# Performance work log

Hardware: AMD Instinct MI355X
Metric: run time of the kernel (lower is better)

The kernel has to match this reference:

```python
import jax, jax.numpy as jnp
import numpy as np

# Mamba2 config fixed by the wrapper: state=32, expand=1, n_groups=1, conv kernel=4
H, P, N, K = 32, 64, 32, 4          # heads, head_dim, state_size, conv kernel
D_MODEL = H * P                      # hidden = intermediate (expand=1) = 2048
CONV_DIM = D_MODEL + 2 * N           # intermediate + 2*n_groups*state = 2112
PROJ = D_MODEL + CONV_DIM + H        # in_proj width = 4192
EPS = 1e-6


def setup_inputs() -> dict:
    key = jax.random.key(0)
    ks = jax.random.split(key, 8)
    B, L = 4, 2048
    w = lambda k, shape, sc=0.02: jax.random.normal(k, shape, jnp.float32) * sc
    return {
        "x": jax.random.normal(ks[0], (B, L, D_MODEL), jnp.float32),
        "W_in": w(ks[1], (D_MODEL, PROJ)),
        "b_in": jnp.zeros((PROJ,), jnp.float32),
        "conv_w": w(ks[2], (CONV_DIM, K), 0.25),
        "conv_b": jnp.zeros((CONV_DIM,), jnp.float32),
        "A_log": jnp.log(jnp.arange(1, H + 1, dtype=jnp.float32)),
        "dt_bias": jax.random.uniform(ks[3], (H,), jnp.float32, -4.0, 0.0),
        "D_param": jnp.ones((H,), jnp.float32),
        "norm_w": jnp.ones((D_MODEL,), jnp.float32),
        "W_out": w(ks[4], (D_MODEL, D_MODEL)),
    }


def reference(x, W_in, b_in, conv_w, conv_b, A_log, dt_bias, D_param, norm_w, W_out):
    B, L, _ = x.shape
    proj = x @ W_in + b_in                                   # (B,L,PROJ)
    gate, hBC, dt_raw = jnp.split(proj, [D_MODEL, D_MODEL + CONV_DIM], axis=-1)

    # causal depthwise conv1d over time (kernel K, left pad K-1), then SiLU
    hp = jnp.pad(hBC, ((0, 0), (K - 1, 0), (0, 0)))
    conv = conv_b + sum(hp[:, k:k + L, :] * conv_w[:, k] for k in range(K))
    conv = jax.nn.silu(conv)

    xs, Bm, Cm = jnp.split(conv, [D_MODEL, D_MODEL + N], axis=-1)
    xs = xs.reshape(B, L, H, P)                              # (B,L,H,P)

    A = -jnp.exp(A_log)                                      # (H,)
    dt = jax.nn.softplus(dt_raw + dt_bias)                   # (B,L,H)
    dA = jnp.exp(dt * A)                                     # (B,L,H)

    def step(hstate, inp):
        dA_t, dt_t, x_t, B_t, C_t = inp                      # (B,H),(B,H),(B,H,P),(B,N),(B,N)
        upd = (dt_t[:, :, None] * x_t)[..., None] * B_t[:, None, None, :]
        hstate = dA_t[:, :, None, None] * hstate + upd       # (B,H,P,N)
        y_t = jnp.einsum('bhpn,bn->bhp', hstate, C_t)
        return hstate, y_t

    h0 = jnp.zeros((B, H, P, N), x.dtype)
    scan_in = (dA.transpose(1, 0, 2), dt.transpose(1, 0, 2),
               xs.transpose(1, 0, 2, 3), Bm.transpose(1, 0, 2), Cm.transpose(1, 0, 2))
    _, ys = jax.lax.scan(step, h0, scan_in)                  # ys: (L,B,H,P)

    y = ys.transpose(1, 0, 2, 3) + D_param[None, None, :, None] * xs
    y = y.reshape(B, L, D_MODEL)

    # gated RMSNorm: gate applied before normalization (MambaRMSNormGated)
    y = y * jax.nn.silu(gate)
    var = jnp.mean(jnp.square(y), axis=-1, keepdims=True)
    y = y * jax.lax.rsqrt(var + EPS) * norm_w
    return y @ W_out
```

## Files before the change

kernel.cpp:

```cpp
#include <hip/hip_runtime.h>
#include <cstdint>
#include <cstddef>

constexpr int kB    = 4;
constexpr int kL    = 2048;
constexpr int kH    = 32;
constexpr int kP    = 64;
constexpr int kN    = 32;
constexpr int kD    = 2048;
constexpr int kProjW = 4192;
constexpr int kLdp  = 4224;
constexpr int kNp1  = 4352;
constexpr int kM    = kB * kL;
constexpr int kK    = kD;
constexpr int kLC   = 128;
constexpr int kNC   = kL / kLC;

typedef _Float16 f16x8 __attribute__((ext_vector_type(8)));
typedef float f32x4 __attribute__((ext_vector_type(4)));

__device__ __forceinline__ float lane_bcast(float v, int lane) {
    return __int_as_float(__builtin_amdgcn_readlane(__float_as_int(v), lane));
}
__device__ __forceinline__ float silu_f(float x) { return x / (1.f + __expf(-x)); }

__device__ __forceinline__ void async_copy16(const void* g, void* lds) {
    __builtin_amdgcn_global_load_lds(
        (const __attribute__((address_space(1))) unsigned int*)(uintptr_t)g,
        (__attribute__((address_space(3))) unsigned int*)(uintptr_t)lds,
        16, 0, 0);
}

__global__ __launch_bounds__(256) void cast_f16_kernel(const float* __restrict__ in,
                                                       _Float16* __restrict__ out) {
    size_t i = ((size_t)blockIdx.x * 256 + threadIdx.x) * 8;
    float4 a = *(const float4*)(in + i);
    float4 b = *(const float4*)(in + i + 4);
    f16x8 o;
    o[0] = (_Float16)a.x; o[1] = (_Float16)a.y; o[2] = (_Float16)a.z; o[3] = (_Float16)a.w;
    o[4] = (_Float16)b.x; o[5] = (_Float16)b.y; o[6] = (_Float16)b.z; o[7] = (_Float16)b.w;
    *(f16x8*)(out + i) = o;
}

__global__ __launch_bounds__(256) void transpose_cast_kernel(const float* __restrict__ W,
                                                             _Float16* __restrict__ Wt,
                                                             int R, int C) {
    __shared__ float tile[32][33];
    const int c0 = blockIdx.x * 32;
    const int r0 = blockIdx.y * 32;
    const int tx = threadIdx.x & 31;
    const int ty = threadIdx.x >> 5;
    #pragma unroll
    for (int i = 0; i < 32; i += 8) {
        int rr = r0 + ty + i;
        int cc = c0 + tx;
        tile[ty + i][tx] = (cc < C) ? W[(size_t)rr * C + cc] : 0.f;
    }
    __syncthreads();
    #pragma unroll
    for (int i = 0; i < 32; i += 8) {
        int cc = c0 + ty + i;
        int rr = r0 + tx;
        Wt[(size_t)cc * R + rr] = (_Float16)tile[tx][ty + i];
    }
}

template <bool OUT_F16>
__global__ __launch_bounds__(512, 2) void gemm256_kernel(
    const _Float16* __restrict__ A, const _Float16* __restrict__ Bt,
    const float* __restrict__ bias, int nbias,
    void* __restrict__ Cout, int K, int ldc, int nvalid, int nn,
    float* __restrict__ dtside)
{
    __shared__ __attribute__((aligned(16))) _Float16 lds[2 * 4 * 8192];

    const int tid = threadIdx.x;
    const int l = tid & 63, r = l & 15, q = l >> 4;
    const int w = tid >> 6, wm = w >> 2, wn = w & 3;

    const int nwg = gridDim.x;
    const int q8 = nwg >> 3;
    const int pid = blockIdx.x;
    const int wg = (pid & 7) * q8 + (pid >> 3);
    const int m_idx = wg / nn;
    const int n_idx = wg - m_idx * nn;
    const size_t tileM = (size_t)m_idx * 256;
    const size_t tileN = (size_t)n_idx * 256;

    const int sR = ((tid >> 7) << 4) | (tid & 15);
    const int sC = ((tid >> 4) & 7) << 3;
    const _Float16* aSrc = A  + (tileM + sR) * (size_t)K + sC;
    const _Float16* bSrc = Bt + (tileN + sR) * (size_t)K + sC;
    _Float16* dst0 = lds + tid * 8;

    auto STAGE = [&](int buf, int part, const _Float16* src, int half, int kt2) {
        const _Float16* s = src + (size_t)(half * 128) * K + kt2 * 64;
        _Float16* d = dst0 + buf * 32768 + part * 8192;
        async_copy16(s, d);
        async_copy16(s + (size_t)64 * K, d + 4096);
    };

    const int NT = K >> 6;
    STAGE(0, 0, aSrc, 0, 0); STAGE(0, 3, bSrc, 1, 0);
    STAGE(0, 1, aSrc, 1, 0); STAGE(0, 2, bSrc, 0, 0);
    STAGE(1, 0, aSrc, 0, 1); STAGE(1, 3, bSrc, 1, 1);
    STAGE(1, 1, aSrc, 1, 1);
    asm volatile("s_waitcnt vmcnt(6)" ::: "memory");
    asm volatile("s_barrier" ::: "memory");

    f32x4 acc[8][4] = {};
    f16x8 afr[4][2], bfr[2][2], bfr2[2][2];

    const int aRd = wm * 4 * 2048 + l * 16;
    const int bRd = wn * 2 * 2048 + l * 16;

#define MFMA_CL(AO, BO, BARR, KK)                                                        \
    _Pragma("unroll")                                                                    \
    for (int i = 0; i < 4; ++i)                                                          \
        _Pragma("unroll")                                                                \
        for (int j = 0; j < 2; ++j)                                                      \
            acc[(AO) + i][(BO) + j] = __builtin_amdgcn_mfma_f32_16x16x32_f16(            \
                afr[i][KK], BARR[j][KK], acc[(AO) + i][(BO) + j], 0, 0, 0);

    for (int kt = 0; kt < NT; ++kt) {
        const int bsel = kt & 1;
        const char* a0 = (const char*)lds + bsel * 65536;
        const char* a1 = a0 + 16384;
        const char* b0 = a0 + 2 * 16384;
        const char* b1 = a0 + 3 * 16384;

        bfr[0][0] = *(const f16x8*)(b0 + bRd);
        bfr[1][0] = *(const f16x8*)(b0 + bRd + 2048);
        afr[0][0] = *(const f16x8*)(a0 + aRd);
        afr[1][0] = *(const f16x8*)(a0 + aRd + 2048);
        afr[2][0] = *(const f16x8*)(a0 + aRd + 4096);
        afr[3][0] = *(const f16x8*)(a0 + aRd + 6144);
        bfr[0][1] = *(const f16x8*)(b0 + bRd + 1024);
        bfr[1][1] = *(const f16x8*)(b0 + bRd + 3072);
        afr[0][1] = *(const f16x8*)(a0 + aRd + 1024);
        afr[1][1] = *(const f16x8*)(a0 + aRd + 3072);
        afr[2][1] = *(const f16x8*)(a0 + aRd + 5120);
        afr[3][1] = *(const f16x8*)(a0 + aRd + 7168);
        if (kt + 1 < NT) STAGE(bsel ^ 1, 2, bSrc, 0, kt + 1);
        asm volatile("s_waitcnt lgkmcnt(6)" ::: "memory");
        __builtin_amdgcn_sched_barrier(0);
        __builtin_amdgcn_s_setprio(1);
        MFMA_CL(0, 0, bfr, 0)
        asm volatile("s_waitcnt lgkmcnt(0)" ::: "memory");
        __builtin_amdgcn_sched_barrier(0);
        MFMA_CL(0, 0, bfr, 1)
        __builtin_amdgcn_s_setprio(0);
        asm volatile("s_barrier" ::: "memory");

        bfr2[0][0] = *(const f16x8*)(b1 + bRd);
        bfr2[1][0] = *(const f16x8*)(b1 + bRd + 2048);
        bfr2[0][1] = *(const f16x8*)(b1 + bRd + 1024);
        bfr2[1][1] = *(const f16x8*)(b1 + bRd + 3072);
        if (kt + 2 < NT) STAGE(bsel, 0, aSrc, 0, kt + 2);
        asm volatile("s_waitcnt lgkmcnt(2)" ::: "memory");
        __builtin_amdgcn_sched_barrier(0);
        __builtin_amdgcn_s_setprio(1);
        MFMA_CL(0, 2, bfr2, 0)
        asm volatile("s_waitcnt lgkmcnt(0)" ::: "memory");
        __builtin_amdgcn_sched_barrier(0);
        MFMA_CL(0, 2, bfr2, 1)
        __builtin_amdgcn_s_setprio(0);
        asm volatile("s_barrier" ::: "memory");

        afr[0][0] = *(const f16x8*)(a1 + aRd);
        afr[1][0] = *(const f16x8*)(a1 + aRd + 2048);
        afr[2][0] = *(const f16x8*)(a1 + aRd + 4096);
        afr[3][0] = *(const f16x8*)(a1 + aRd + 6144);
        afr[0][1] = *(const f16x8*)(a1 + aRd + 1024);
        afr[1][1] = *(const f16x8*)(a1 + aRd + 3072);
        afr[2][1] = *(const f16x8*)(a1 + aRd + 5120);
        afr[3][1] = *(const f16x8*)(a1 + aRd + 7168);
        if (kt + 2 < NT) STAGE(bsel, 3, bSrc, 1, kt + 2);
        asm volatile("s_waitcnt lgkmcnt(4)" ::: "memory");
        __builtin_amdgcn_sched_barrier(0);
        __builtin_amdgcn_s_setprio(1);
        MFMA_CL(4, 2, bfr2, 0)
        asm volatile("s_waitcnt lgkmcnt(0)" ::: "memory");
        __builtin_amdgcn_sched_barrier(0);
        MFMA_CL(4, 2, bfr2, 1)
        __builtin_amdgcn_s_setprio(0);
        asm volatile("s_barrier" ::: "memory");

        if (kt + 2 < NT) STAGE(bsel, 1, aSrc, 1, kt + 2);
        __builtin_amdgcn_s_setprio(1);
        MFMA_CL(4, 0, bfr, 0)
        MFMA_CL(4, 0, bfr, 1)
        __builtin_amdgcn_s_setprio(0);
        if (kt + 2 < NT) asm volatile("s_waitcnt vmcnt(6)" ::: "memory");
        else             asm volatile("s_waitcnt vmcnt(0)" ::: "memory");
        asm volatile("s_barrier" ::: "memory");
    }
#undef MFMA_CL

    #pragma unroll
    for (int bb = 0; bb < 4; ++bb) {
        const int nh = bb >> 1, j = bb & 1;
        const int col = (int)tileN + nh * 128 + wn * 32 + j * 16 + r;
        if (col >= nvalid) continue;
        float bv = 0.f;
        if (bias != nullptr && col < nbias) bv = bias[col];
        #pragma unroll
        for (int aa = 0; aa < 8; ++aa) {
            const int mh = aa >> 2, i = aa & 3;
            const size_t row = tileM + (size_t)(mh * 128 + wm * 64 + i * 16 + q * 4);
            #pragma unroll
            for (int u = 0; u < 4; ++u) {
                float v = acc[aa][bb][u] + bv;
                if (OUT_F16) ((_Float16*)Cout)[(row + u) * (size_t)ldc + col] = (_Float16)v;
                else         ((float*)Cout)[(row + u) * (size_t)ldc + col] = v;
                if (dtside != nullptr && col >= 4160 && col < 4192)
                    dtside[(row + u) * 32 + (col - 4160)] = v;
            }
        }
    }
}

__global__ __launch_bounds__(256) void dt_da_kernel(
    const float* __restrict__ dtraw, const float* __restrict__ A_log,
    const float* __restrict__ dt_bias, float* __restrict__ dtv, float* __restrict__ dAv)
{
    int idx = blockIdx.x * 256 + threadIdx.x;
    int t  = idx & (kL - 1);
    int bh = idx >> 11;
    int h  = bh & (kH - 1);
    int b  = bh >> 5;
    float z  = dtraw[((size_t)(b * kL + t)) * kH + h] + dt_bias[h];
    float dt = (z > 20.f) ? z : log1pf(expf(z));
    float dA = expf(dt * -expf(A_log[h]));
    dtv[idx] = dt;
    dAv[idx] = dA;
}

__global__ __launch_bounds__(64) void scan_pass1_kernel(
    const _Float16* __restrict__ projh, const float* __restrict__ conv_w,
    const float* __restrict__ conv_b, const float* __restrict__ dtv,
    const float* __restrict__ dAv, float* __restrict__ cstate, float* __restrict__ Pch)
{
    const int blk = blockIdx.x;
    const int c   = blk & (kNC - 1);
    const int bh  = blk >> 4;
    const int h   = bh & (kH - 1);
    const int b   = bh >> 5;
    const int l   = threadIdx.x;
    const int t0  = c * kLC;

    const int chx = h * kP + l;
    const int chb = 2048 + (l & 31);
    const float xw0 = conv_w[chx*4+0], xw1 = conv_w[chx*4+1], xw2 = conv_w[chx*4+2], xw3 = conv_w[chx*4+3];
    const float xbb = conv_b[chx];
    const float bw0 = conv_w[chb*4+0], bw1 = conv_w[chb*4+1], bw2 = conv_w[chb*4+2], bw3 = conv_w[chb*4+3];
    const float bbb = conv_b[chb];

    const _Float16* pb = projh + (size_t)b * kL * kLdp;
    const int colx = 2048 + chx;
    const int colb = 2048 + chb;

    float xq0=0.f, xq1=0.f, xq2=0.f, bq0=0.f, bq1=0.f, bq2=0.f;
    if (c > 0) {
        xq0 = (float)pb[(size_t)(t0-3)*kLdp + colx];
        xq1 = (float)pb[(size_t)(t0-2)*kLdp + colx];
        xq2 = (float)pb[(size_t)(t0-1)*kLdp + colx];
        bq0 = (float)pb[(size_t)(t0-3)*kLdp + colb];
        bq1 = (float)pb[(size_t)(t0-2)*kLdp + colb];
        bq2 = (float)pb[(size_t)(t0-1)*kLdp + colb];
    }

    float hs[kN];
    #pragma unroll
    for (int n = 0; n < kN; ++n) hs[n] = 0.f;
    float Pp = 1.f;
    const float* dtp = dtv + (size_t)bh * kL;
    const float* dAp = dAv + (size_t)bh * kL;

    #pragma unroll 1
    for (int t = t0; t < t0 + kLC; ++t) {
        const size_t ro = (size_t)t * kLdp;
        float xv = (float)pb[ro + colx];
        float bv = (float)pb[ro + colb];
        float sx = silu_f(xbb + xw0*xq0 + xw1*xq1 + xw2*xq2 + xw3*xv);
        float sb = silu_f(bbb + bw0*bq0 + bw1*bq1 + bw2*bq2 + bw3*bv);
        xq0=xq1; xq1=xq2; xq2=xv;
        bq0=bq1; bq1=bq2; bq2=bv;
        float dt = dtp[t], dA = dAp[t];
        float dtx = dt * sx;
        Pp *= dA;
        #pragma unroll
        for (int n = 0; n < kN; ++n)
            hs[n] = fmaf(dA, hs[n], dtx * lane_bcast(sb, n));
    }
    float* cs = cstate + (size_t)blk * (kP * kN) + l * kN;
    #pragma unroll
    for (int n = 0; n < kN; ++n) cs[n] = hs[n];
    if (l == 0) Pch[blk] = Pp;
}

__global__ __launch_bounds__(256) void scan_pass2_kernel(float* __restrict__ cstate,
                                                         const float* __restrict__ Pch) {
    const int bh  = blockIdx.x;
    const int off = threadIdx.x * 8;
    float s[8];
    #pragma unroll
    for (int i = 0; i < 8; ++i) s[i] = 0.f;
    float* base = cstate + (size_t)bh * (kNC * kP * kN) + off;
    #pragma unroll 1
    for (int c = 0; c < kNC; ++c) {
        float* cs = base + c * (kP * kN);
        float Pp = Pch[bh * kNC + c];
        #pragma unroll
        for (int i = 0; i < 8; ++i) {
            float loc = cs[i];
            cs[i] = s[i];
            s[i] = fmaf(Pp, s[i], loc);
        }
    }
}

__global__ __launch_bounds__(64) void scan_pass3_kernel(
    const _Float16* __restrict__ projh, const float* __restrict__ conv_w,
    const float* __restrict__ conv_b, const float* __restrict__ dtv,
    const float* __restrict__ dAv, const float* __restrict__ cstate,
    const float* __restrict__ D_param, float* __restrict__ ypre)
{
    const int blk = blockIdx.x;
    const int c   = blk & (kNC - 1);
    const int bh  = blk >> 4;
    const int h   = bh & (kH - 1);
    const int b   = bh >> 5;
    const int l   = threadIdx.x;
    const int t0  = c * kLC;

    const int chx = h * kP + l;
    const int chc = 2048 + l;
    const float xw0 = conv_w[chx*4+0], xw1 = conv_w[chx*4+1], xw2 = conv_w[chx*4+2], xw3 = conv_w[chx*4+3];
    const float xbb = conv_b[chx];
    const float cw0 = conv_w[chc*4+0], cw1 = conv_w[chc*4+1], cw2 = conv_w[chc*4+2], cw3 = conv_w[chc*4+3];
    const float cbb = conv_b[chc];

    const _Float16* pb = projh + (size_t)b * kL * kLdp;
    const int colx = 2048 + chx;
    const int colc = 2048 + chc;

    float xq0=0.f, xq1=0.f, xq2=0.f, cq0=0.f, cq1=0.f, cq2=0.f;
    if (c > 0) {
        xq0 = (float)pb[(size_t)(t0-3)*kLdp + colx];
        xq1 = (float)pb[(size_t)(t0-2)*kLdp + colx];
        xq2 = (float)pb[(size_t)(t0-1)*kLdp + colx];
        cq0 = (float)pb[(size_t)(t0-3)*kLdp + colc];
        cq1 = (float)pb[(size_t)(t0-2)*kLdp + colc];
        cq2 = (float)pb[(size_t)(t0-1)*kLdp + colc];
    }

    float hs[kN];
    const float* cs = cstate + (size_t)blk * (kP * kN) + l * kN;
    #pragma unroll
    for (int n = 0; n < kN; ++n) hs[n] = cs[n];
    const float Dh = D_param[h];
    const float* dtp = dtv + (size_t)bh * kL;
    const float* dAp = dAv + (size_t)bh * kL;
    float* yo = ypre + (size_t)b * kL * kD + h * kP + l;

    #pragma unroll 1
    for (int t = t0; t < t0 + kLC; ++t) {
        const size_t ro = (size_t)t * kLdp;
        float xv = (float)pb[ro + colx];
        float cv = (float)pb[ro + colc];
        float sx = silu_f(xbb + xw0*xq0 + xw1*xq1 + xw2*xq2 + xw3*xv);
        float sc = silu_f(cbb + cw0*cq0 + cw1*cq1 + cw2*cq2 + cw3*cv);
        xq0=xq1; xq1=xq2; xq2=xv;
        cq0=cq1; cq1=cq2; cq2=cv;
        float dt = dtp[t], dA = dAp[t];
        float dtx = dt * sx;
        float y0 = Dh * sx, y1 = 0.f;
        #pragma unroll
        for (int n = 0; n < kN; ++n) {
            float bn = lane_bcast(sc, n);
            float cn = lane_bcast(sc, n + 32);
            hs[n] = fmaf(dA, hs[n], dtx * bn);
            if (n & 1) y1 = fmaf(hs[n], cn, y1);
            else       y0 = fmaf(hs[n], cn, y0);
        }
        yo[(size_t)t * kD] = y0 + y1;
    }
}

__global__ __launch_bounds__(256) void gated_norm_kernel(
    const float* __restrict__ ypre, const _Float16* __restrict__ projh,
    const float* __restrict__ norm_w, _Float16* __restrict__ yh)
{
    const int row = blockIdx.x;
    const int tid = threadIdx.x;
    const float* yr = ypre + (size_t)row * kD;
    const _Float16* gr = projh + (size_t)row * kLdp;
    float v[8];
    float ss = 0.f;
    #pragma unroll
    for (int u = 0; u < 8; ++u) {
        int col = tid + u * 256;
        float g = (float)gr[col];
        float t = yr[col] * (g / (1.f + __expf(-g)));
        v[u] = t;
        ss = fmaf(t, t, ss);
    }
    #pragma unroll
    for (int off = 32; off > 0; off >>= 1) ss += __shfl_xor(ss, off, 64);
    __shared__ float red[4];
    if ((tid & 63) == 0) red[tid >> 6] = ss;
    __syncthreads();
    float tot = (red[0] + red[1]) + (red[2] + red[3]);
    float scl = rsqrtf(tot * (1.f / (float)kD) + 1e-6f);
    #pragma unroll
    for (int u = 0; u < 8; ++u) {
        int col = tid + u * 256;
        yh[(size_t)row * kD + col] = (_Float16)(v[u] * scl * norm_w[col]);
    }
}

extern "C" void kernel_launch(void* const* d_in, const int* in_sizes, int n_in,
                              void* d_out, int out_size, void* d_ws, size_t ws_size,
                              hipStream_t stream)
{
    (void)in_sizes; (void)n_in; (void)out_size; (void)ws_size;
    const float* x       = (const float*)d_in[0];
    const float* W_in    = (const float*)d_in[1];
    const float* b_in    = (const float*)d_in[2];
    const float* conv_w  = (const float*)d_in[3];
    const float* conv_b  = (const float*)d_in[4];
    const float* A_log   = (const float*)d_in[5];
    const float* dt_bias = (const float*)d_in[6];
    const float* D_param = (const float*)d_in[7];
    const float* norm_w  = (const float*)d_in[8];
    const float* W_out   = (const float*)d_in[9];
    float* out = (float*)d_out;

    char* p = (char*)d_ws;
    _Float16* projh = (_Float16*)p; p += (size_t)kM * kLdp * 2;
    _Float16* xh    = (_Float16*)p; p += (size_t)kM * kD * 2;
    _Float16* Wt    = (_Float16*)p; p += (size_t)kNp1 * kK * 2;
    _Float16* Wot   = (_Float16*)p; p += (size_t)kD * kK * 2;
    float* dtraw    = (float*)p;    p += (size_t)kM * kH * 4;
    float* dtv      = (float*)p;    p += (size_t)kB * kH * kL * 4;
    float* dAv      = (float*)p;    p += (size_t)kB * kH * kL * 4;
    float* cstate   = (float*)p;    p += (size_t)kB * kH * kNC * kP * kN * 4;
    float* Pch      = (float*)p;    p += (size_t)kB * kH * kNC * 4;
    _Float16* yh = xh;
    float* ypre = out;

    cast_f16_kernel<<<(kM * kD) / (256 * 8), 256, 0, stream>>>(x, xh);
    transpose_cast_kernel<<<dim3(kNp1 / 32, kK / 32), 256, 0, stream>>>(W_in, Wt, kK, kProjW);
    transpose_cast_kernel<<<dim3(kD / 32, kK / 32), 256, 0, stream>>>(W_out, Wot, kK, kD);
    gemm256_kernel<true><<<(kM / 256) * (kNp1 / 256), 512, 0, stream>>>(
        xh, Wt, b_in, kProjW, (void*)projh, kK, kLdp, kLdp, kNp1 / 256, dtraw);
    dt_da_kernel<<<(kB * kH * kL) / 256, 256, 0, stream>>>(dtraw, A_log, dt_bias, dtv, dAv);
    scan_pass1_kernel<<<kB * kH * kNC, 64, 0, stream>>>(projh, conv_w, conv_b, dtv, dAv, cstate, Pch);
    scan_pass2_kernel<<<kB * kH, 256, 0, stream>>>(cstate, Pch);
    scan_pass3_kernel<<<kB * kH * kNC, 64, 0, stream>>>(projh, conv_w, conv_b, dtv, dAv, cstate, D_param, ypre);
    gated_norm_kernel<<<kM, 256, 0, stream>>>(ypre, projh, norm_w, yh);
    gemm256_kernel<false><<<(kM / 256) * (kD / 256), 512, 0, stream>>>(
        yh, Wot, nullptr, 0, (void*)out, kK, kD, kD, kD / 256, nullptr);
}
```

Measured before the change: 726.7 us.

## Split in_proj GEMM into main and tail kernels, retune scan chunks and GEMM pipeline

Splits the input projection GEMM into a 4096-column main GEMM (no padded 256-tile for the last 96 columns) and a small tail GEMM that also computes dt/dA, removing the separate dt_da kernel and the dtraw buffer. It restructures the main GEMM's K-loop staging and barrier schedule, halves the scan chunk length to double scan parallelism, prefetches next-timestep inputs in the scan passes, and aliases cstate onto the xh workspace. The risks are less overlap from the coarser waits, the tail GEMM becoming a low-occupancy serial step, and workspace aliasing hazards.

```diff
diff --git a/kernel.cpp b/kernel.cpp
--- a/kernel.cpp
+++ b/kernel.cpp
@@ -10,10 +10,9 @@
 constexpr int kD    = 2048;
 constexpr int kProjW = 4192;
 constexpr int kLdp  = 4224;
-constexpr int kNp1  = 4352;
 constexpr int kM    = kB * kL;
 constexpr int kK    = kD;
-constexpr int kLC   = 128;
+constexpr int kLC   = 64;
 constexpr int kNC   = kL / kLC;
 
 typedef _Float16 f16x8 __attribute__((ext_vector_type(8)));
@@ -69,8 +68,7 @@
 __global__ __launch_bounds__(512, 2) void gemm256_kernel(
     const _Float16* __restrict__ A, const _Float16* __restrict__ Bt,
     const float* __restrict__ bias, int nbias,
-    void* __restrict__ Cout, int K, int ldc, int nvalid, int nn,
-    float* __restrict__ dtside)
+    void* __restrict__ Cout, int K, int ldc, int nvalid, int nn)
 {
     __shared__ __attribute__((aligned(16))) _Float16 lds[2 * 4 * 8192];
 
@@ -100,12 +98,11 @@
         async_copy16(s + (size_t)64 * K, d + 4096);
     };
 
-    const int NT = K >> 6;
-    STAGE(0, 0, aSrc, 0, 0); STAGE(0, 3, bSrc, 1, 0);
-    STAGE(0, 1, aSrc, 1, 0); STAGE(0, 2, bSrc, 0, 0);
+    const int NT = K >> 5 >> 1;
+    STAGE(0, 0, aSrc, 0, 0); STAGE(0, 1, aSrc, 1, 0);
+    STAGE(0, 2, bSrc, 0, 0); STAGE(0, 3, bSrc, 1, 0);
     STAGE(1, 0, aSrc, 0, 1); STAGE(1, 3, bSrc, 1, 1);
-    STAGE(1, 1, aSrc, 1, 1);
-    asm volatile("s_waitcnt vmcnt(6)" ::: "memory");
+    asm volatile("s_waitcnt vmcnt(4)" ::: "memory");
     asm volatile("s_barrier" ::: "memory");
 
     f32x4 acc[8][4] = {};
@@ -124,74 +121,65 @@
 
     for (int kt = 0; kt < NT; ++kt) {
         const int bsel = kt & 1;
-        const char* a0 = (const char*)lds + bsel * 65536;
-        const char* a1 = a0 + 16384;
-        const char* b0 = a0 + 2 * 16384;
-        const char* b1 = a0 + 3 * 16384;
-
-        bfr[0][0] = *(const f16x8*)(b0 + bRd);
-        bfr[1][0] = *(const f16x8*)(b0 + bRd + 2048);
-        afr[0][0] = *(const f16x8*)(a0 + aRd);
-        afr[1][0] = *(const f16x8*)(a0 + aRd + 2048);
-        afr[2][0] = *(const f16x8*)(a0 + aRd + 4096);
-        afr[3][0] = *(const f16x8*)(a0 + aRd + 6144);
-        bfr[0][1] = *(const f16x8*)(b0 + bRd + 1024);
-        bfr[1][1] = *(const f16x8*)(b0 + bRd + 3072);
-        afr[0][1] = *(const f16x8*)(a0 + aRd + 1024);
-        afr[1][1] = *(const f16x8*)(a0 + aRd + 3072);
-        afr[2][1] = *(const f16x8*)(a0 + aRd + 5120);
-        afr[3][1] = *(const f16x8*)(a0 + aRd + 7168);
-        if (kt + 1 < NT) STAGE(bsel ^ 1, 2, bSrc, 0, kt + 1);
-        asm volatile("s_waitcnt lgkmcnt(6)" ::: "memory");
+        const char* a0p = (const char*)lds + bsel * 65536;
+        const char* a1p = a0p + 16384;
+        const char* b0p = a0p + 2 * 16384;
+        const char* b1p = a0p + 3 * 16384;
+
+        afr[0][0] = *(const f16x8*)(a0p + aRd);
+        afr[1][0] = *(const f16x8*)(a0p + aRd + 2048);
+        afr[2][0] = *(const f16x8*)(a0p + aRd + 4096);
+        afr[3][0] = *(const f16x8*)(a0p + aRd + 6144);
+        afr[0][1] = *(const f16x8*)(a0p + aRd + 1024);
+        afr[1][1] = *(const f16x8*)(a0p + aRd + 3072);
+        afr[2][1] = *(const f16x8*)(a0p + aRd + 5120);
+        afr[3][1] = *(const f16x8*)(a0p + aRd + 7168);
+        bfr[0][0] = *(const f16x8*)(b0p + bRd);
+        bfr[1][0] = *(const f16x8*)(b0p + bRd + 2048);
+        bfr[0][1] = *(const f16x8*)(b0p + bRd + 1024);
+        bfr[1][1] = *(const f16x8*)(b0p + bRd + 3072);
+        __builtin_amdgcn_sched_barrier(0);
+        bfr2[0][0] = *(const f16x8*)(b1p + bRd);
+        bfr2[1][0] = *(const f16x8*)(b1p + bRd + 2048);
+        bfr2[0][1] = *(const f16x8*)(b1p + bRd + 1024);
+        bfr2[1][1] = *(const f16x8*)(b1p + bRd + 3072);
+        if (kt + 1 < NT) {
+            STAGE(bsel ^ 1, 2, bSrc, 0, kt + 1);
+            STAGE(bsel ^ 1, 1, aSrc, 1, kt + 1);
+        }
+        asm volatile("s_waitcnt lgkmcnt(4)" ::: "memory");
         __builtin_amdgcn_sched_barrier(0);
         __builtin_amdgcn_s_setprio(1);
         MFMA_CL(0, 0, bfr, 0)
+        MFMA_CL(0, 0, bfr, 1)
         asm volatile("s_waitcnt lgkmcnt(0)" ::: "memory");
         __builtin_amdgcn_sched_barrier(0);
-        MFMA_CL(0, 0, bfr, 1)
-        __builtin_amdgcn_s_setprio(0);
-        asm volatile("s_barrier" ::: "memory");
-
-        bfr2[0][0] = *(const f16x8*)(b1 + bRd);
-        bfr2[1][0] = *(const f16x8*)(b1 + bRd + 2048);
-        bfr2[0][1] = *(const f16x8*)(b1 + bRd + 1024);
-        bfr2[1][1] = *(const f16x8*)(b1 + bRd + 3072);
-        if (kt + 2 < NT) STAGE(bsel, 0, aSrc, 0, kt + 2);
-        asm volatile("s_waitcnt lgkmcnt(2)" ::: "memory");
-        __builtin_amdgcn_sched_barrier(0);
-        __builtin_amdgcn_s_setprio(1);
         MFMA_CL(0, 2, bfr2, 0)
-        asm volatile("s_waitcnt lgkmcnt(0)" ::: "memory");
-        __builtin_amdgcn_sched_barrier(0);
         MFMA_CL(0, 2, bfr2, 1)
         __builtin_amdgcn_s_setprio(0);
+
+        afr[0][0] = *(const f16x8*)(a1p + aRd);
+        afr[1][0] = *(const f16x8*)(a1p + aRd + 2048);
+        afr[2][0] = *(const f16x8*)(a1p + aRd + 4096);
+        afr[3][0] = *(const f16x8*)(a1p + aRd + 6144);
+        afr[0][1] = *(const f16x8*)(a1p + aRd + 1024);
+        afr[1][1] = *(const f16x8*)(a1p + aRd + 3072);
+        afr[2][1] = *(const f16x8*)(a1p + aRd + 5120);
+        afr[3][1] = *(const f16x8*)(a1p + aRd + 7168);
         asm volatile("s_barrier" ::: "memory");
-
-        afr[0][0] = *(const f16x8*)(a1 + aRd);
-        afr[1][0] = *(const f16x8*)(a1 + aRd + 2048);
-        afr[2][0] = *(const f16x8*)(a1 + aRd + 4096);
-        afr[3][0] = *(const f16x8*)(a1 + aRd + 6144);
-        afr[0][1] = *(const f16x8*)(a1 + aRd + 1024);
-        afr[1][1] = *(const f16x8*)(a1 + aRd + 3072);
-        afr[2][1] = *(const f16x8*)(a1 + aRd + 5120);
-        afr[3][1] = *(const f16x8*)(a1 + aRd + 7168);
-        if (kt + 2 < NT) STAGE(bsel, 3, bSrc, 1, kt + 2);
-        asm volatile("s_waitcnt lgkmcnt(4)" ::: "memory");
+        if (kt + 2 < NT) {
+            STAGE(bsel, 0, aSrc, 0, kt + 2);
+            STAGE(bsel, 3, bSrc, 1, kt + 2);
+        }
+        asm volatile("s_waitcnt lgkmcnt(0)" ::: "memory");
         __builtin_amdgcn_sched_barrier(0);
         __builtin_amdgcn_s_setprio(1);
         MFMA_CL(4, 2, bfr2, 0)
-        asm volatile("s_waitcnt lgkmcnt(0)" ::: "memory");
-        __builtin_amdgcn_sched_barrier(0);
         MFMA_CL(4, 2, bfr2, 1)
-        __builtin_amdgcn_s_setprio(0);
-        asm volatile("s_barrier" ::: "memory");
-
-        if (kt + 2 < NT) STAGE(bsel, 1, aSrc, 1, kt + 2);
-        __builtin_amdgcn_s_setprio(1);
         MFMA_CL(4, 0, bfr, 0)
         MFMA_CL(4, 0, bfr, 1)
         __builtin_amdgcn_s_setprio(0);
-        if (kt + 2 < NT) asm volatile("s_waitcnt vmcnt(6)" ::: "memory");
+        if (kt + 2 < NT) asm volatile("s_waitcnt vmcnt(4)" ::: "memory");
         else             asm volatile("s_waitcnt vmcnt(0)" ::: "memory");
         asm volatile("s_barrier" ::: "memory");
     }
@@ -213,27 +201,109 @@
                 float v = acc[aa][bb][u] + bv;
                 if (OUT_F16) ((_Float16*)Cout)[(row + u) * (size_t)ldc + col] = (_Float16)v;
                 else         ((float*)Cout)[(row + u) * (size_t)ldc + col] = v;
-                if (dtside != nullptr && col >= 4160 && col < 4192)
-                    dtside[(row + u) * 32 + (col - 4160)] = v;
             }
         }
     }
 }
 
-__global__ __launch_bounds__(256) void dt_da_kernel(
-    const float* __restrict__ dtraw, const float* __restrict__ A_log,
-    const float* __restrict__ dt_bias, float* __restrict__ dtv, float* __restrict__ dAv)
+__global__ __launch_bounds__(256) void gemm_tail_kernel(
+    const _Float16* __restrict__ A, const _Float16* __restrict__ Bt,
+    const float* __restrict__ bias , _Float16* __restrict__ Cout,
+    const float* __restrict__ A_log, const float* __restrict__ dt_bias,
+    float* __restrict__ dtv, float* __restrict__ dAv)
 {
-    int idx = blockIdx.x * 256 + threadIdx.x;
-    int t  = idx & (kL - 1);
-    int bh = idx >> 11;
-    int h  = bh & (kH - 1);
-    int b  = bh >> 5;
-    float z  = dtraw[((size_t)(b * kL + t)) * kH + h] + dt_bias[h];
-    float dt = (z > 20.f) ? z : log1pf(expf(z));
-    float dA = expf(dt * -expf(A_log[h]));
-    dtv[idx] = dt;
-    dAv[idx] = dA;
+    __shared__ __attribute__((aligned(16))) _Float16 lds[2 * 10240];
+    const int K = kK;
+    const int tid = threadIdx.x;
+    const int l = tid & 63, r = l & 15, q = l >> 4;
+    const int w = tid >> 6;
+    const size_t tileM = (size_t)blockIdx.x * 32;
+
+    const int sRa = ((tid >> 7) << 4) | (tid & 15);
+    const int sC  = ((tid >> 4) & 7) << 3;
+    const _Float16* aSrc = A + (tileM + sRa) * (size_t)K + sC;
+    const _Float16* bSrc = Bt + (size_t)sRa * K + sC;
+    _Float16* dst0 = lds + tid * 8;
+
+    auto STG = [&](int buf, int kt2) {
+        const _Float16* a = aSrc + kt2 * 64;
+        const _Float16* b = bSrc + kt2 * 64;
+        _Float16* d = dst0 + buf * 10240;
+        async_copy16(a, d);
+        #pragma unroll
+        for (int c = 0; c < 4; ++c)
+            async_copy16(b + (size_t)(c * 32) * K, d + 2048 + c * 2048);
+    };
+
+    const int NT = K / 64;
+    STG(0, 0); STG(1, 1);
+    asm volatile("s_waitcnt vmcnt(5)" ::: "memory");
+    asm volatile("s_barrier" ::: "memory");
+
+    f32x4 acc[2][2] = {};
+    f16x8 af[2][2], bf[2][2];
+    const int aRdT = l * 16;
+    const int bRdT = 4096 + w * 2 * 2048 + l * 16;
+
+    for (int kt = 0; kt < NT; ++kt) {
+        const char* base = (const char*)lds + (kt & 1) * 20480;
+        af[0][0] = *(const f16x8*)(base + aRdT);
+        af[1][0] = *(const f16x8*)(base + aRdT + 2048);
+        af[0][1] = *(const f16x8*)(base + aRdT + 1024);
+        af[1][1] = *(const f16x8*)(base + aRdT + 3072);
+        bf[0][0] = *(const f16x8*)(base + bRdT);
+        bf[1][0] = *(const f16x8*)(base + bRdT + 2048);
+        bf[0][1] = *(const f16x8*)(base + bRdT + 1024);
+        bf[1][1] = *(const f16x8*)(base + bRdT + 3072);
+        asm volatile("s_waitcnt lgkmcnt(0)" ::: "memory");
+        __builtin_amdgcn_sched_barrier(0);
+        asm volatile("s_barrier" ::: "memory");
+        if (kt + 2 < NT) STG(kt & 1, kt + 2);
+        #pragma unroll
+        for (int kk = 0; kk < 2; ++kk)
+            #pragma unroll
+            for (int i = 0; i < 2; ++i)
+                #pragma unroll
+                for (int j = 0; j < 2; ++j)
+                    acc[i][j] = __builtin_amdgcn_mfma_f32_16x16x32_f16(af[i][kk], bf[j][kk], acc[i][j], 0, 0, 0);
+        if (kt + 2 < NT) asm volatile("s_waitcnt vmcnt(5)" ::: "memory");
+        else             asm volatile("s_waitcnt vmcnt(0)" ::: "memory");
+        asm volatile("s_barrier" ::: "memory");
+    }
+
+    #pragma unroll
+    for (int j = 0; j < 2; ++j) {
+        const int colOff = w * 32 + j * 16 + r;
+        const float bv = (colOff < 96) ? bias[colOff] : 0.f;
+        #pragma unroll
+        for (int i = 0; i < 2; ++i) {
+            #pragma unroll
+            for (int u = 0; u < 4; ++u) {
+                const size_t row = tileM + (size_t)(i * 16 + q * 4 + u);
+                float v = acc[i][j][u] + bv;
+                Cout[row * kLdp + 4096 + colOff] = (_Float16)v;
+            }
+        }
+        if (colOff >= 64 && colOff < 96) {
+            const int h = colOff - 64;
+            const float db = dt_bias[h];
+            const float nA = -expf(A_log[h]);
+            #pragma unroll
+            for (int i = 0; i < 2; ++i) {
+                #pragma unroll
+                for (int u = 0; u < 4; ++u) {
+                    const size_t row = tileM + (size_t)(i * 16 + q * 4 + u);
+                    const int b = (int)(row >> 11), t = (int)(row & 2047);
+                    float z = acc[i][j][u] + bv + db;
+                    float dt = (z > 20.f) ? z : log1pf(expf(z));
+                    float dA = expf(dt * nA);
+                    const size_t idx = (((size_t)b * kH + h) << 11) | t;
+                    dtv[idx] = dt;
+                    dAv[idx] = dA;
+                }
+            }
+        }
+    }
 }
 
 __global__ __launch_bounds__(64) void scan_pass1_kernel(
@@ -243,7 +313,7 @@
 {
     const int blk = blockIdx.x;
     const int c   = blk & (kNC - 1);
-    const int bh  = blk >> 4;
+    const int bh  = blk >> 5;
     const int h   = bh & (kH - 1);
     const int b   = bh >> 5;
     const int l   = threadIdx.x;
@@ -277,21 +347,29 @@
     const float* dtp = dtv + (size_t)bh * kL;
     const float* dAp = dAv + (size_t)bh * kL;
 
+    float xv = (float)pb[(size_t)t0 * kLdp + colx];
+    float bv = (float)pb[(size_t)t0 * kLdp + colb];
+    float dt = dtp[t0], dA = dAp[t0];
+
     #pragma unroll 1
     for (int t = t0; t < t0 + kLC; ++t) {
-        const size_t ro = (size_t)t * kLdp;
-        float xv = (float)pb[ro + colx];
-        float bv = (float)pb[ro + colb];
+        float xn = 0.f, bn = 0.f, dtn = 0.f, dAn = 0.f;
+        if (t + 1 < t0 + kLC) {
+            const size_t ro2 = (size_t)(t + 1) * kLdp;
+            xn = (float)pb[ro2 + colx];
+            bn = (float)pb[ro2 + colb];
+            dtn = dtp[t + 1]; dAn = dAp[t + 1];
+        }
         float sx = silu_f(xbb + xw0*xq0 + xw1*xq1 + xw2*xq2 + xw3*xv);
         float sb = silu_f(bbb + bw0*bq0 + bw1*bq1 + bw2*bq2 + bw3*bv);
         xq0=xq1; xq1=xq2; xq2=xv;
         bq0=bq1; bq1=bq2; bq2=bv;
-        float dt = dtp[t], dA = dAp[t];
         float dtx = dt * sx;
         Pp *= dA;
         #pragma unroll
         for (int n = 0; n < kN; ++n)
             hs[n] = fmaf(dA, hs[n], dtx * lane_bcast(sb, n));
+        xv = xn; bv = bn; dt = dtn; dA = dAn;
     }
     float* cs = cstate + (size_t)blk * (kP * kN) + l * kN;
     #pragma unroll
@@ -328,7 +406,7 @@
 {
     const int blk = blockIdx.x;
     const int c   = blk & (kNC - 1);
-    const int bh  = blk >> 4;
+    const int bh  = blk >> 5;
     const int h   = bh & (kH - 1);
     const int b   = bh >> 5;
     const int l   = threadIdx.x;
@@ -364,16 +442,23 @@
     const float* dAp = dAv + (size_t)bh * kL;
     float* yo = ypre + (size_t)b * kL * kD + h * kP + l;
 
+    float xv = (float)pb[(size_t)t0 * kLdp + colx];
+    float cv = (float)pb[(size_t)t0 * kLdp + colc];
+    float dt = dtp[t0], dA = dAp[t0];
+
     #pragma unroll 1
     for (int t = t0; t < t0 + kLC; ++t) {
-        const size_t ro = (size_t)t * kLdp;
-        float xv = (float)pb[ro + colx];
-        float cv = (float)pb[ro + colc];
+        float xn = 0.f, cn2 = 0.f, dtn = 0.f, dAn = 0.f;
+        if (t + 1 < t0 + kLC) {
+            const size_t ro2 = (size_t)(t + 1) * kLdp;
+            xn = (float)pb[ro2 + colx];
+            cn2 = (float)pb[ro2 + colc];
+            dtn = dtp[t + 1]; dAn = dAp[t + 1];
+        }
         float sx = silu_f(xbb + xw0*xq0 + xw1*xq1 + xw2*xq2 + xw3*xv);
         float sc = silu_f(cbb + cw0*cq0 + cw1*cq1 + cw2*cq2 + cw3*cv);
         xq0=xq1; xq1=xq2; xq2=xv;
         cq0=cq1; cq1=cq2; cq2=cv;
-        float dt = dtp[t], dA = dAp[t];
         float dtx = dt * sx;
         float y0 = Dh * sx, y1 = 0.f;
         #pragma unroll
@@ -385,6 +470,7 @@
             else       y0 = fmaf(hs[n], cn, y0);
         }
         yo[(size_t)t * kD] = y0 + y1;
+        xv = xn; cv = cn2; dt = dtn; dA = dAn;
     }
 }
 
@@ -440,26 +526,26 @@
     char* p = (char*)d_ws;
     _Float16* projh = (_Float16*)p; p += (size_t)kM * kLdp * 2;
     _Float16* xh    = (_Float16*)p; p += (size_t)kM * kD * 2;
-    _Float16* Wt    = (_Float16*)p; p += (size_t)kNp1 * kK * 2;
+    _Float16* Wt    = (_Float16*)p; p += (size_t)kLdp * kK * 2;
     _Float16* Wot   = (_Float16*)p; p += (size_t)kD * kK * 2;
-    float* dtraw    = (float*)p;    p += (size_t)kM * kH * 4;
     float* dtv      = (float*)p;    p += (size_t)kB * kH * kL * 4;
     float* dAv      = (float*)p;    p += (size_t)kB * kH * kL * 4;
-    float* cstate   = (float*)p;    p += (size_t)kB * kH * kNC * kP * kN * 4;
     float* Pch      = (float*)p;    p += (size_t)kB * kH * kNC * 4;
-    _Float16* yh = xh;
+    float* cstate = (float*)xh;
+    _Float16* yh  = xh;
     float* ypre = out;
 
     cast_f16_kernel<<<(kM * kD) / (256 * 8), 256, 0, stream>>>(x, xh);
-    transpose_cast_kernel<<<dim3(kNp1 / 32, kK / 32), 256, 0, stream>>>(W_in, Wt, kK, kProjW);
+    transpose_cast_kernel<<<dim3(kLdp / 32, kK / 32), 256, 0, stream>>>(W_in, Wt, kK, kProjW);
     transpose_cast_kernel<<<dim3(kD / 32, kK / 32), 256, 0, stream>>>(W_out, Wot, kK, kD);
-    gemm256_kernel<true><<<(kM / 256) * (kNp1 / 256), 512, 0, stream>>>(
-        xh, Wt, b_in, kProjW, (void*)projh, kK, kLdp, kLdp, kNp1 / 256, dtraw);
-    dt_da_kernel<<<(kB * kH * kL) / 256, 256, 0, stream>>>(dtraw, A_log, dt_bias, dtv, dAv);
+    gemm256_kernel<true><<<512, 512, 0, stream>>>(
+        xh, Wt, b_in, kProjW, (void*)projh, kK, kLdp, 4096, 16);
+    gemm_tail_kernel<<<kM / 32, 256, 0, stream>>>(
+        xh, Wt + (size_t)4096 * kK, b_in + 4096, projh, A_log, dt_bias, dtv, dAv);
     scan_pass1_kernel<<<kB * kH * kNC, 64, 0, stream>>>(projh, conv_w, conv_b, dtv, dAv, cstate, Pch);
     scan_pass2_kernel<<<kB * kH, 256, 0, stream>>>(cstate, Pch);
     scan_pass3_kernel<<<kB * kH * kNC, 64, 0, stream>>>(projh, conv_w, conv_b, dtv, dAv, cstate, D_param, ypre);
     gated_norm_kernel<<<kM, 256, 0, stream>>>(ypre, projh, norm_w, yh);
-    gemm256_kernel<false><<<(kM / 256) * (kD / 256), 512, 0, stream>>>(
-        yh, Wot, nullptr, 0, (void*)out, kK, kD, kD, kD / 256, nullptr);
-}
+    gemm256_kernel<false><<<256, 512, 0, stream>>>(
+        yh, Wot, nullptr, 0, (void*)out, kK, kD, kD, 8);
+}
```

After: 620.2 us. 1.17x faster.
